# Performance work log

Measured on AMD Instinct MI355X. Metric: run time of the kernel, lower is better.

Reference implementation:

```python
import jax, jax.numpy as jnp
import numpy as np

# config constants
B, S, H = 4, 2048, 1024
E = 8                 # n_routed_experts
M = 512               # moe_intermediate_size
K = 2                 # num_experts_per_tok
N_SHARED = 2
SM = M * N_SHARED     # shared expert intermediate
G = 64                # gene_size
GE_TEMP = 1.0
ALPHA = 0.001         # aux_loss_alpha
SEQ_AUX = True
NORM_TOPK = True
COS_TEMP = 0.78
CONS_ALPHA = 0.01
LEAKY_SLOPE = 0.01
EPS_COS = 1e-8


def setup_inputs() -> dict:
    key = jax.random.key(0)
    ks = jax.random.split(key, 12)
    sh = 1.0 / np.sqrt(H)
    sm = 1.0 / np.sqrt(M)
    ssm = 1.0 / np.sqrt(SM)
    sg = 1.0 / np.sqrt(G)
    return {
        "hidden_states": jax.random.normal(ks[0], (B, S, H), jnp.float32),
        "g": jax.random.normal(ks[1], (B, G), jnp.float32),
        "wt": jax.random.uniform(ks[2], (E, H), jnp.float32, -sh, sh),   # gate weight_token
        "wg": jax.random.uniform(ks[3], (E, G), jnp.float32, -sg, sg),   # gate weight_gene
        "w_gate": jax.random.uniform(ks[4], (E, H, M), jnp.float32, -sh, sh),
        "w_up": jax.random.uniform(ks[5], (E, H, M), jnp.float32, -sh, sh),
        "w_down": jax.random.uniform(ks[6], (E, M, H), jnp.float32, -sm, sm),
        "sw_gate": jax.random.uniform(ks[7], (H, SM), jnp.float32, -sh, sh),
        "sw_up": jax.random.uniform(ks[8], (H, SM), jnp.float32, -sh, sh),
        "sw_down": jax.random.uniform(ks[9], (SM, H), jnp.float32, -ssm, ssm),
    }


def _leaky(x):
    return jnp.where(x >= 0, x, LEAKY_SLOPE * x)


def _moe_forward(hidden_states, g, wt, wg, w_gate, w_up, w_down, sw_gate, sw_up, sw_down):
    b, s, h = hidden_states.shape
    x = hidden_states.reshape(-1, h)                    # [T, H], T = b*s
    T = x.shape[0]

    # ---- gate ----
    logits_h = x @ wt.T                                 # [T, E]
    logits_g = g @ wg.T                                 # [b, E]
    logits_g = jnp.repeat(logits_g, s, axis=0)          # [T, E]
    logits = (logits_h + logits_g / GE_TEMP) / (1.0 + 1.0 / GE_TEMP)
    scores = jax.nn.softmax(logits, axis=-1)            # [T, E]
    topk_w, topk_idx = jax.lax.top_k(scores, K)         # [T, K]
    if K > 1 and NORM_TOPK:
        topk_w = topk_w / (topk_w.sum(-1, keepdims=True) + 1e-20)

    # aux loss (seq_aux=True)
    onehot = jax.nn.one_hot(topk_idx.reshape(b, s * K), E, dtype=jnp.float32)  # [b, s*K, E]
    ce = onehot.sum(1) / (s * K / E)                    # [b, E]
    aux_loss = (ce * scores.reshape(b, s, E).mean(1)).sum(1).mean() * ALPHA

    # ---- routed experts: dense stacked compute, then gather ----
    gp = _leaky(jnp.einsum('th,ehm->etm', x, w_gate))   # [E, T, M]
    up = jnp.einsum('th,ehm->etm', x, w_up)
    y_all = jnp.einsum('etm,emh->eth', gp * up, w_down) # [E, T, H]
    y_sel = y_all[topk_idx, jnp.arange(T)[:, None], :]  # [T, K, H]
    y = (y_sel * topk_w[..., None]).sum(1).reshape(b, s, h)

    # ---- shared expert ----
    p = (_leaky(hidden_states @ sw_gate) * (hidden_states @ sw_up)) @ sw_down
    y = y + p

    # consistency cosine loss
    num = jnp.sum(y * p, -1)
    den = jnp.maximum(jnp.linalg.norm(y, axis=-1), EPS_COS) * jnp.maximum(jnp.linalg.norm(p, axis=-1), EPS_COS)
    closs = CONS_ALPHA * jnp.mean((num / den) / (1.0 + COS_TEMP))
    return y, aux_loss + closs


def reference(hidden_states, g, wt, wg, w_gate, w_up, w_down, sw_gate, sw_up, sw_down):
    y, _ = _moe_forward(hidden_states, g, wt, wg, w_gate, w_up, w_down, sw_gate, sw_up, sw_down)
    return y
```

## Files before the change

### kernel.cpp

```cpp
#include <hip/hip_runtime.h>
#include <stdint.h>

#define T_TOK 8192
#define H_DIM 1024
#define M_DIM 512
#define SM_DIM 1024
#define E_NUM 8
#define S_SEQ 2048
#define G_DIM 64
#define NASSIGN 16384
#define NSLOT (NASSIGN + E_NUM * 256)
#define MAX_TILES (NASSIGN / 256 + E_NUM)
#define NBLK_PLACE (NASSIGN / 256)

typedef float f32x4 __attribute__((ext_vector_type(4)));
typedef short bf16x8 __attribute__((ext_vector_type(8)));

struct TileDesc { int base; int expert; int nrows; };

#define WAITCNT_VM6 asm volatile("s_waitcnt vmcnt(6)" ::: "memory")
#define WAITCNT_VM4 asm volatile("s_waitcnt vmcnt(4)" ::: "memory")
#define WAITCNT_VM2 asm volatile("s_waitcnt vmcnt(2)" ::: "memory")
#define WAITCNT_VM0 asm volatile("s_waitcnt vmcnt(0)" ::: "memory")
#define WAITCNT_LGKM0 asm volatile("s_waitcnt lgkmcnt(0)" ::: "memory")

static __device__ __forceinline__ ushort f2b(float f) {
  union { float f; uint32_t u; } a; a.f = f;
  uint32_t r = a.u + 0x7fffu + ((a.u >> 16) & 1u);
  return (ushort)(r >> 16);
}
static __device__ __forceinline__ float b2f(ushort u) {
  union { uint32_t u; float f; } a; a.u = ((uint32_t)u) << 16;
  return a.f;
}
static __device__ __forceinline__ int imin(int a, int b) { return a < b ? a : b; }

static __device__ __forceinline__ void gll16(const void* g, void* l) {
  __builtin_amdgcn_global_load_lds(
      (const __attribute__((address_space(1))) void*)g,
      (__attribute__((address_space(3))) void*)l, 16, 0, 0);
}
static __device__ __forceinline__ int xcd_remap(int wg, int nwg) {
  return (wg & 7) * (nwg >> 3) + (wg >> 3);
}

__global__ void cvt_x_kernel(const float* __restrict__ x, ushort* __restrict__ xb) {
  int i = blockIdx.x * 256 + threadIdx.x;
  const float4 v = ((const float4*)x)[i];
  ushort4 o;
  o.x = f2b(v.x); o.y = f2b(v.y); o.z = f2b(v.z); o.w = f2b(v.w);
  ((ushort4*)xb)[i] = o;
}

__global__ void tcvt_kernel(const float* __restrict__ src, ushort* __restrict__ dst, int R, int C) {
  __shared__ float tile[32][33];
  size_t bo = (size_t)blockIdx.z * R * C;
  src += bo; dst += bo;
  int c0 = blockIdx.x * 32, r0 = blockIdx.y * 32;
#pragma unroll
  for (int i = 0; i < 4; ++i)
    tile[threadIdx.y + i * 8][threadIdx.x] =
        src[(size_t)(r0 + threadIdx.y + i * 8) * C + c0 + threadIdx.x];
  __syncthreads();
#pragma unroll
  for (int i = 0; i < 4; ++i)
    dst[(size_t)(c0 + threadIdx.y + i * 8) * R + r0 + threadIdx.x] =
        f2b(tile[threadIdx.x][threadIdx.y + i * 8]);
}

__global__ void lg_kernel(const float* __restrict__ g, const float* __restrict__ wg,
                          float* __restrict__ lg) {
  int tid = threadIdx.x;
  if (tid < 4 * E_NUM) {
    int b = tid >> 3, e = tid & 7;
    float s = 0.f;
    for (int i = 0; i < G_DIM; ++i) s += g[b * G_DIM + i] * wg[e * G_DIM + i];
    lg[tid] = s;
  }
}

__global__ __launch_bounds__(64) void router_kernel(
    const float* __restrict__ x, const float* __restrict__ wt, const float* __restrict__ lg,
    int* __restrict__ tidx, float* __restrict__ tw) {
  int t = blockIdx.x;
  int lane = threadIdx.x;
  const float* xr = x + (size_t)t * H_DIM;
  float a[E_NUM];
#pragma unroll
  for (int e = 0; e < E_NUM; ++e) a[e] = 0.f;
  for (int i = lane; i < H_DIM; i += 64) {
    float xv = xr[i];
#pragma unroll
    for (int e = 0; e < E_NUM; ++e) a[e] += xv * wt[e * H_DIM + i];
  }
#pragma unroll
  for (int e = 0; e < E_NUM; ++e)
    for (int off = 32; off; off >>= 1) a[e] += __shfl_xor(a[e], off, 64);
  if (lane == 0) {
    int b = t / S_SEQ;
    float l[E_NUM];
#pragma unroll
    for (int e = 0; e < E_NUM; ++e) l[e] = 0.5f * (a[e] + lg[b * E_NUM + e]);
    int i1 = 0; float b1 = l[0];
#pragma unroll
    for (int e = 1; e < E_NUM; ++e) if (l[e] > b1) { b1 = l[e]; i1 = e; }
    int i2 = -1; float b2 = -1e30f;
#pragma unroll
    for (int e = 0; e < E_NUM; ++e) if (e != i1 && l[e] > b2) { b2 = l[e]; i2 = e; }
    float e2 = expf(b2 - b1);
    float inv = 1.f / (1.f + e2);
    tidx[t * 2] = i1; tidx[t * 2 + 1] = i2;
    tw[t * 2] = inv;  tw[t * 2 + 1] = e2 * inv;
  }
}

__global__ __launch_bounds__(256) void hist_kernel(const int* __restrict__ tidx,
                                                   int* __restrict__ bcount) {
  __shared__ int h[E_NUM];
  int tid = threadIdx.x;
  if (tid < E_NUM) h[tid] = 0;
  __syncthreads();
  atomicAdd(&h[tidx[blockIdx.x * 256 + tid]], 1);
  __syncthreads();
  if (tid < E_NUM) bcount[blockIdx.x * E_NUM + tid] = h[tid];
}

__global__ __launch_bounds__(64) void scan2_kernel(
    const int* __restrict__ bcount, int* __restrict__ boffs, int* __restrict__ offs,
    TileDesc* __restrict__ desc, int* __restrict__ ndesc) {
  __shared__ int cnt[E_NUM];
  __shared__ int off_s[E_NUM];
  int lane = threadIdx.x;
  if (lane < E_NUM) {
    int s = 0;
    for (int b = 0; b < NBLK_PLACE; ++b) s += bcount[b * E_NUM + lane];
    cnt[lane] = s;
  }
  __syncthreads();
  if (lane == 0) {
    int o = 0, nd = 0;
    for (int e = 0; e < E_NUM; ++e) {
      off_s[e] = o;
      offs[e] = o;
      int n = cnt[e];
      for (int tb = 0; tb < n; tb += 256) {
        desc[nd].base = o + tb; desc[nd].expert = e;
        desc[nd].nrows = imin(n - tb, 256);
        ++nd;
      }
      o += n;
    }
    offs[E_NUM] = o;
    *ndesc = nd;
  }
  __syncthreads();
  if (lane < E_NUM) {
    int run = off_s[lane];
    for (int b = 0; b < NBLK_PLACE; ++b) {
      boffs[b * E_NUM + lane] = run;
      run += bcount[b * E_NUM + lane];
    }
  }
}

__global__ __launch_bounds__(256) void place2_kernel(
    const int* __restrict__ tidx, const int* __restrict__ boffs,
    int* __restrict__ perm, int* __restrict__ slot_of) {
  __shared__ int wcnt[4][E_NUM];
  int tid = threadIdx.x, wv = tid >> 6, lane = tid & 63;
  int i = blockIdx.x * 256 + tid;
  int e = tidx[i];
  unsigned long long lower = (lane == 63) ? 0x7fffffffffffffffull : ((1ull << lane) - 1ull);
  int rank = 0;
#pragma unroll
  for (int ee = 0; ee < E_NUM; ++ee) {
    unsigned long long m = __ballot(e == ee);
    if (e == ee) rank = __popcll(m & lower);
    if (lane == 0) wcnt[wv][ee] = __popcll(m);
  }
  __syncthreads();
  int off = boffs[blockIdx.x * E_NUM + e];
  for (int w = 0; w < wv; ++w) off += wcnt[w][e];
  int pos = off + rank;
  perm[pos] = i >> 1;
  slot_of[i] = pos;
}

template <int DUAL>
static __device__ __forceinline__ void gemm_core8(
    const ushort* __restrict__ A, const ushort* __restrict__ B0,
    const ushort* __restrict__ B1, void* __restrict__ Out, int outf32,
    int Kd, int NdOut, int rowbase, int nrows, int n0,
    const int* __restrict__ perm, ushort* __restrict__ LDS) {
  int tid = threadIdx.x, wv = tid >> 6, lane = tid & 63;
  int wr = wv >> 2, wc = wv & 3;
  int lr = lane & 15, cg = lane >> 4;
  int sid = lane >> 3, dch = lane & 7;

  const ushort* apA[2][2];
  const ushort* apB[2][2];
#pragma unroll
  for (int qm = 0; qm < 2; ++qm)
#pragma unroll
    for (int k = 0; k < 2; ++k) {
      int idx = k * 64 + wv * 8 + sid;
      int gch = dch ^ (idx & 7);
      int grow = (idx >> 6) * 128 + qm * 64 + (idx & 63);
      grow = imin(grow, nrows - 1);
      int arow = perm ? perm[rowbase + grow] : rowbase + grow;
      apA[qm][k] = A + (size_t)arow * Kd + gch * 8;
    }
#pragma unroll
  for (int qn = 0; qn < 2; ++qn)
#pragma unroll
    for (int k = 0; k < 2; ++k) {
      int idx = k * 64 + wv * 8 + sid;
      int gch = dch ^ (idx & 7);
      int vrow = n0 + (idx >> 5) * 64 + qn * 32 + (idx & 31);
      const ushort* src; int brow;
      if (DUAL) {
        src = ((vrow >> 4) & 1) ? B1 : B0;
        brow = (vrow >> 5) * 16 + (vrow & 15);
      } else {
        src = B0; brow = vrow;
      }
      apB[qn][k] = src + (size_t)brow * Kd + gch * 8;
    }

  auto stgA = [&](int qm, int k, int nd) {
    gll16(apA[qm][k], LDS + nd * 16384 + qm * 8192 + (k * 512 + wv * 64) * 8);
    apA[qm][k] += 64;
  };
  auto stgB = [&](int qn, int k, int nd) {
    gll16(apB[qn][k], LDS + 32768 + nd * 16384 + qn * 8192 + (k * 512 + wv * 64) * 8);
    apB[qn][k] += 64;
  };
  auto rdA = [&](int d, int qm, int m, int kk) -> bf16x8 {
    int idx = wr * 64 + m * 16 + lr;
    int ch = (kk * 4 + cg) ^ (idx & 7);
    return *(const bf16x8*)(LDS + d * 16384 + qm * 8192 + idx * 64 + ch * 8);
  };
  auto rdB = [&](int d, int qn, int n, int kk) -> bf16x8 {
    int idx = wc * 32 + n * 16 + lr;
    int ch = (kk * 4 + cg) ^ (idx & 7);
    return *(const bf16x8*)(LDS + 32768 + d * 16384 + qn * 8192 + idx * 64 + ch * 8);
  };

  f32x4 acc[2][2][4][2];
#pragma unroll
  for (int qm = 0; qm < 2; ++qm)
#pragma unroll
    for (int qn = 0; qn < 2; ++qn)
#pragma unroll
      for (int m = 0; m < 4; ++m)
#pragma unroll
        for (int n = 0; n < 2; ++n) acc[qm][qn][m][n] = (f32x4){0.f, 0.f, 0.f, 0.f};

  int nk = Kd >> 6;
  stgA(0, 0, 0); stgA(0, 1, 0);
  stgB(0, 0, 0); stgB(0, 1, 0);
  stgB(1, 0, 0); stgB(1, 1, 0);
  stgA(1, 0, 0); stgA(1, 1, 0);
  WAITCNT_VM4;
  __builtin_amdgcn_s_barrier();

  for (int t = 0; t < nk; ++t) {
    int cur = t & 1, nxt = cur ^ 1;
    bool hn = (t + 1 < nk);
    bf16x8 a0f[4][2], a1f[4][2], b0f[2][2], b1f[2][2];

#pragma unroll
    for (int m = 0; m < 4; ++m) { a0f[m][0] = rdA(cur, 0, m, 0); a0f[m][1] = rdA(cur, 0, m, 1); }
#pragma unroll
    for (int n = 0; n < 2; ++n) { b0f[n][0] = rdB(cur, 0, n, 0); b0f[n][1] = rdB(cur, 0, n, 1); }
    if (hn) { stgA(0, 0, nxt); stgA(0, 1, nxt); WAITCNT_VM4; } else { WAITCNT_VM2; }
    WAITCNT_LGKM0;
    __builtin_amdgcn_s_barrier();
    __builtin_amdgcn_s_setprio(1);
#pragma unroll
    for (int m = 0; m < 4; ++m)
#pragma unroll
      for (int n = 0; n < 2; ++n) {
        acc[0][0][m][n] = __builtin_amdgcn_mfma_f32_16x16x32_bf16(a0f[m][0], b0f[n][0], acc[0][0][m][n], 0, 0, 0);
        acc[0][0][m][n] = __builtin_amdgcn_mfma_f32_16x16x32_bf16(a0f[m][1], b0f[n][1], acc[0][0][m][n], 0, 0, 0);
      }
    __builtin_amdgcn_s_setprio(0);

#pragma unroll
    for (int n = 0; n < 2; ++n) { b1f[n][0] = rdB(cur, 1, n, 0); b1f[n][1] = rdB(cur, 1, n, 1); }
    if (hn) { stgB(0, 0, nxt); stgB(0, 1, nxt); WAITCNT_VM4; } else { WAITCNT_VM0; }
    WAITCNT_LGKM0;
    __builtin_amdgcn_s_barrier();
    __builtin_amdgcn_s_setprio(1);
#pragma unroll
    for (int m = 0; m < 4; ++m)
#pragma unroll
      for (int n = 0; n < 2; ++n) {
        acc[0][1][m][n] = __builtin_amdgcn_mfma_f32_16x16x32_bf16(a0f[m][0], b1f[n][0], acc[0][1][m][n], 0, 0, 0);
        acc[0][1][m][n] = __builtin_amdgcn_mfma_f32_16x16x32_bf16(a0f[m][1], b1f[n][1], acc[0][1][m][n], 0, 0, 0);
      }
    __builtin_amdgcn_s_setprio(0);

#pragma unroll
    for (int m = 0; m < 4; ++m) { a1f[m][0] = rdA(cur, 1, m, 0); a1f[m][1] = rdA(cur, 1, m, 1); }
    if (hn) { stgB(1, 0, nxt); stgB(1, 1, nxt); WAITCNT_VM6; }
    WAITCNT_LGKM0;
    __builtin_amdgcn_s_barrier();
    __builtin_amdgcn_s_setprio(1);
#pragma unroll
    for (int m = 0; m < 4; ++m)
#pragma unroll
      for (int n = 0; n < 2; ++n) {
        acc[1][0][m][n] = __builtin_amdgcn_mfma_f32_16x16x32_bf16(a1f[m][0], b0f[n][0], acc[1][0][m][n], 0, 0, 0);
        acc[1][0][m][n] = __builtin_amdgcn_mfma_f32_16x16x32_bf16(a1f[m][1], b0f[n][1], acc[1][0][m][n], 0, 0, 0);
      }
    __builtin_amdgcn_s_setprio(0);

    if (hn) { stgA(1, 0, nxt); stgA(1, 1, nxt); WAITCNT_VM4; }
    WAITCNT_LGKM0;
    __builtin_amdgcn_s_barrier();
    __builtin_amdgcn_s_setprio(1);
#pragma unroll
    for (int m = 0; m < 4; ++m)
#pragma unroll
      for (int n = 0; n < 2; ++n) {
        acc[1][1][m][n] = __builtin_amdgcn_mfma_f32_16x16x32_bf16(a1f[m][0], b1f[n][0], acc[1][1][m][n], 0, 0, 0);
        acc[1][1][m][n] = __builtin_amdgcn_mfma_f32_16x16x32_bf16(a1f[m][1], b1f[n][1], acc[1][1][m][n], 0, 0, 0);
      }
    __builtin_amdgcn_s_setprio(0);
  }

#pragma unroll
  for (int qm = 0; qm < 2; ++qm)
#pragma unroll
    for (int qn = 0; qn < 2; ++qn)
#pragma unroll
      for (int m = 0; m < 4; ++m)
#pragma unroll
        for (int r = 0; r < 4; ++r) {
          int row = wr * 128 + qm * 64 + m * 16 + cg * 4 + r;
          if (row < nrows) {
            if (DUAL) {
              float gv = acc[qm][qn][m][0][r], uv = acc[qm][qn][m][1][r];
              float hv = (gv >= 0.f ? gv : 0.01f * gv) * uv;
              int col = ((n0 >> 5) + wc * 2 + qn) * 16 + lr;
              ((ushort*)Out)[(size_t)(rowbase + row) * NdOut + col] = f2b(hv);
            } else {
#pragma unroll
              for (int n = 0; n < 2; ++n) {
                int col = n0 + wc * 64 + qn * 32 + n * 16 + lr;
                size_t o = (size_t)(rowbase + row) * NdOut + col;
                if (outf32) ((float*)Out)[o] = acc[qm][qn][m][n][r];
                else ((ushort*)Out)[o] = f2b(acc[qm][qn][m][n][r]);
              }
            }
          }
        }
}

__global__ __launch_bounds__(512) void gemm_dual_all(
    const ushort* __restrict__ xb, const ushort* __restrict__ swg,
    const ushort* __restrict__ swu, ushort* __restrict__ hsh,
    const ushort* __restrict__ wg, const ushort* __restrict__ wu,
    ushort* __restrict__ h_e, const int* __restrict__ perm,
    const TileDesc* __restrict__ desc, const int* __restrict__ ndesc) {
  __shared__ ushort LDS[65536];
  int id = xcd_remap(blockIdx.x, gridDim.x);
  if (id < 256) {
    int mt = id >> 3, n0 = (id & 7) * 256;
    gemm_core8<1>(xb, swg, swu, hsh, 0, H_DIM, SM_DIM, mt * 256, 256, n0, nullptr, LDS);
  } else {
    int rid = id - 256;
    int mt = rid >> 2, n0 = (rid & 3) * 256;
    if (mt >= *ndesc) return;
    TileDesc d = desc[mt];
    size_t wo = (size_t)d.expert * M_DIM * H_DIM;
    gemm_core8<1>(xb, wg + wo, wu + wo, h_e, 0, H_DIM, M_DIM, d.base, d.nrows, n0, perm, LDS);
  }
}

__global__ __launch_bounds__(512) void gemm_down_all(
    const ushort* __restrict__ hsh, const ushort* __restrict__ swd, float* __restrict__ y,
    const ushort* __restrict__ h_e, const ushort* __restrict__ wd, ushort* __restrict__ ye,
    const TileDesc* __restrict__ desc, const int* __restrict__ ndesc) {
  __shared__ ushort LDS[65536];
  int id = xcd_remap(blockIdx.x, gridDim.x);
  if (id < 128) {
    int mt = id >> 2, n0 = (id & 3) * 256;
    gemm_core8<0>(hsh, swd, nullptr, (void*)y, 1, SM_DIM, H_DIM, mt * 256, 256, n0, nullptr, LDS);
  } else {
    int rid = id - 128;
    int mt = rid >> 2, n0 = (rid & 3) * 256;
    if (mt >= *ndesc) return;
    TileDesc d = desc[mt];
    gemm_core8<0>(h_e, wd + (size_t)d.expert * H_DIM * M_DIM, nullptr, (void*)ye, 0,
                  M_DIM, H_DIM, d.base, d.nrows, n0, nullptr, LDS);
  }
}

__global__ void final_kernel(float* __restrict__ y, const ushort* __restrict__ ye,
                             const int* __restrict__ slot_of, const float* __restrict__ tw) {
  int i = blockIdx.x * 256 + threadIdx.x;
  int t = i >> 8;
  int c4 = (i & 255) * 4;
  int s0 = slot_of[t * 2], s1 = slot_of[t * 2 + 1];
  float w0 = tw[t * 2], w1 = tw[t * 2 + 1];
  float4 v = ((float4*)y)[i];
  ushort4 a = *(const ushort4*)(ye + (size_t)s0 * H_DIM + c4);
  ushort4 b = *(const ushort4*)(ye + (size_t)s1 * H_DIM + c4);
  v.x += w0 * b2f(a.x) + w1 * b2f(b.x);
  v.y += w0 * b2f(a.y) + w1 * b2f(b.y);
  v.z += w0 * b2f(a.z) + w1 * b2f(b.z);
  v.w += w0 * b2f(a.w) + w1 * b2f(b.w);
  ((float4*)y)[i] = v;
}

extern "C" void kernel_launch(void* const* d_in, const int* in_sizes, int n_in,
                              void* d_out, int out_size, void* d_ws, size_t ws_size,
                              hipStream_t stream) {
  const float* x       = (const float*)d_in[0];
  const float* g       = (const float*)d_in[1];
  const float* wt      = (const float*)d_in[2];
  const float* wg      = (const float*)d_in[3];
  const float* w_gate  = (const float*)d_in[4];
  const float* w_up    = (const float*)d_in[5];
  const float* w_down  = (const float*)d_in[6];
  const float* sw_gate = (const float*)d_in[7];
  const float* sw_up   = (const float*)d_in[8];
  const float* sw_down = (const float*)d_in[9];
  float* y = (float*)d_out;

  char* p = (char*)d_ws;
  auto alloc = [&](size_t bytes) -> char* {
    char* r = p;
    p += (bytes + 255) & ~(size_t)255;
    return r;
  };
  ushort* xb    = (ushort*)alloc((size_t)T_TOK * H_DIM * 2);
  ushort* wg_t  = (ushort*)alloc((size_t)E_NUM * M_DIM * H_DIM * 2);
  ushort* wu_t  = (ushort*)alloc((size_t)E_NUM * M_DIM * H_DIM * 2);
  ushort* wd_t  = (ushort*)alloc((size_t)E_NUM * H_DIM * M_DIM * 2);
  ushort* swg_t = (ushort*)alloc((size_t)SM_DIM * H_DIM * 2);
  ushort* swu_t = (ushort*)alloc((size_t)SM_DIM * H_DIM * 2);
  ushort* swd_t = (ushort*)alloc((size_t)H_DIM * SM_DIM * 2);
  float* lg     = (float*)alloc(4 * E_NUM * 4);
  int* tidx     = (int*)alloc(NASSIGN * 4);
  float* tw     = (float*)alloc(NASSIGN * 4);
  int* bcount   = (int*)alloc(NBLK_PLACE * E_NUM * 4);
  int* boffs    = (int*)alloc(NBLK_PLACE * E_NUM * 4);
  int* offs     = (int*)alloc((E_NUM + 1) * 4);
  int* ndesc    = (int*)alloc(4);
  int* perm     = (int*)alloc(NASSIGN * 4);
  int* slot_of  = (int*)alloc(NASSIGN * 4);
  TileDesc* desc = (TileDesc*)alloc(MAX_TILES * sizeof(TileDesc));
  ushort* h_e   = (ushort*)alloc((size_t)NSLOT * M_DIM * 2);
  ushort* hsh   = (ushort*)alloc((size_t)T_TOK * SM_DIM * 2);
  ushort* ye    = (ushort*)alloc((size_t)NSLOT * H_DIM * 2);
  (void)ws_size; (void)in_sizes; (void)n_in; (void)out_size;

  cvt_x_kernel<<<T_TOK * H_DIM / 4 / 256, 256, 0, stream>>>(x, xb);
  dim3 tb(32, 8);
  tcvt_kernel<<<dim3(M_DIM / 32, H_DIM / 32, E_NUM), tb, 0, stream>>>(w_gate, wg_t, H_DIM, M_DIM);
  tcvt_kernel<<<dim3(M_DIM / 32, H_DIM / 32, E_NUM), tb, 0, stream>>>(w_up, wu_t, H_DIM, M_DIM);
  tcvt_kernel<<<dim3(H_DIM / 32, M_DIM / 32, E_NUM), tb, 0, stream>>>(w_down, wd_t, M_DIM, H_DIM);
  tcvt_kernel<<<dim3(SM_DIM / 32, H_DIM / 32, 1), tb, 0, stream>>>(sw_gate, swg_t, H_DIM, SM_DIM);
  tcvt_kernel<<<dim3(SM_DIM / 32, H_DIM / 32, 1), tb, 0, stream>>>(sw_up, swu_t, H_DIM, SM_DIM);
  tcvt_kernel<<<dim3(H_DIM / 32, SM_DIM / 32, 1), tb, 0, stream>>>(sw_down, swd_t, SM_DIM, H_DIM);

  lg_kernel<<<1, 32, 0, stream>>>(g, wg, lg);
  router_kernel<<<T_TOK, 64, 0, stream>>>(x, wt, lg, tidx, tw);
  hist_kernel<<<NBLK_PLACE, 256, 0, stream>>>(tidx, bcount);
  scan2_kernel<<<1, 64, 0, stream>>>(bcount, boffs, offs, desc, ndesc);
  place2_kernel<<<NBLK_PLACE, 256, 0, stream>>>(tidx, boffs, perm, slot_of);

  gemm_dual_all<<<256 + MAX_TILES * 4, 512, 0, stream>>>(
      xb, swg_t, swu_t, hsh, wg_t, wu_t, h_e, perm, desc, ndesc);
  gemm_down_all<<<128 + MAX_TILES * 4, 512, 0, stream>>>(
      hsh, swd_t, y, h_e, wd_t, ye, desc, ndesc);

  final_kernel<<<T_TOK * H_DIM / 4 / 256, 256, 0, stream>>>(y, ye, slot_of, tw);
}
```

Before: 222.2 us.

## Fuse weight/x conversion and routing into one prep kernel, bf16 shared output

Merges the six weight transpose-convert launches, the x-to-bf16 conversion, the gene-logit kernel and the router into a single prep kernel. The router now reads x once with float4 loads and writes the bf16 copy in the same pass. The shared-expert down projection now writes a bf16 buffer instead of the fp32 output. The final kernel uses a grid-stride loop to sum the shared and routed results and write y. This cuts launch overhead and the extra fp32 read-modify-write of y, at the cost of rounding the shared-expert output to bf16 and recomputing the gene logits in every wave.

```diff
diff --git a/kernel.cpp b/kernel.cpp
--- a/kernel.cpp
+++ b/kernel.cpp
@@ -44,63 +44,76 @@
   return (wg & 7) * (nwg >> 3) + (wg >> 3);
 }
 
-__global__ void cvt_x_kernel(const float* __restrict__ x, ushort* __restrict__ xb) {
-  int i = blockIdx.x * 256 + threadIdx.x;
-  const float4 v = ((const float4*)x)[i];
-  ushort4 o;
-  o.x = f2b(v.x); o.y = f2b(v.y); o.z = f2b(v.z); o.w = f2b(v.w);
-  ((ushort4*)xb)[i] = o;
-}
-
-__global__ void tcvt_kernel(const float* __restrict__ src, ushort* __restrict__ dst, int R, int C) {
+__global__ __launch_bounds__(256) void prep_kernel(
+    const float* __restrict__ x, const float* __restrict__ wt, const float* __restrict__ g,
+    const float* __restrict__ wgm,
+    const float* __restrict__ w_gate, const float* __restrict__ w_up,
+    const float* __restrict__ w_down, const float* __restrict__ sw_gate,
+    const float* __restrict__ sw_up, const float* __restrict__ sw_down,
+    ushort* __restrict__ wg_t, ushort* __restrict__ wu_t,
+    ushort* __restrict__ wd_t, ushort* __restrict__ swg_t,
+    ushort* __restrict__ swu_t, ushort* __restrict__ swd_t,
+    ushort* __restrict__ xb, int* __restrict__ tidx, float* __restrict__ tw) {
   __shared__ float tile[32][33];
-  size_t bo = (size_t)blockIdx.z * R * C;
-  src += bo; dst += bo;
-  int c0 = blockIdx.x * 32, r0 = blockIdx.y * 32;
-#pragma unroll
-  for (int i = 0; i < 4; ++i)
-    tile[threadIdx.y + i * 8][threadIdx.x] =
-        src[(size_t)(r0 + threadIdx.y + i * 8) * C + c0 + threadIdx.x];
-  __syncthreads();
-#pragma unroll
-  for (int i = 0; i < 4; ++i)
-    dst[(size_t)(c0 + threadIdx.y + i * 8) * R + r0 + threadIdx.x] =
-        f2b(tile[threadIdx.x][threadIdx.y + i * 8]);
-}
-
-__global__ void lg_kernel(const float* __restrict__ g, const float* __restrict__ wg,
-                          float* __restrict__ lg) {
-  int tid = threadIdx.x;
-  if (tid < 4 * E_NUM) {
-    int b = tid >> 3, e = tid & 7;
-    float s = 0.f;
-    for (int i = 0; i < G_DIM; ++i) s += g[b * G_DIM + i] * wg[e * G_DIM + i];
-    lg[tid] = s;
-  }
-}
-
-__global__ __launch_bounds__(64) void router_kernel(
-    const float* __restrict__ x, const float* __restrict__ wt, const float* __restrict__ lg,
-    int* __restrict__ tidx, float* __restrict__ tw) {
-  int t = blockIdx.x;
-  int lane = threadIdx.x;
-  const float* xr = x + (size_t)t * H_DIM;
+  int id = blockIdx.x;
+  if (id < 15360) {
+    int tx = threadIdx.x & 31, ty = threadIdx.x >> 5;
+    const float* src; ushort* dst; int R, C, t;
+    if (id < 4096)        { src = w_gate;  dst = wg_t;  R = 1024; C = 512;  t = id; }
+    else if (id < 8192)   { src = w_up;    dst = wu_t;  R = 1024; C = 512;  t = id - 4096; }
+    else if (id < 12288)  { src = w_down;  dst = wd_t;  R = 512;  C = 1024; t = id - 8192; }
+    else if (id < 13312)  { src = sw_gate; dst = swg_t; R = 1024; C = 1024; t = id - 12288; }
+    else if (id < 14336)  { src = sw_up;   dst = swu_t; R = 1024; C = 1024; t = id - 13312; }
+    else                  { src = sw_down; dst = swd_t; R = 1024; C = 1024; t = id - 14336; }
+    int tc = C >> 5;
+    int tpm = (R >> 5) * tc;
+    int e = t / tpm, tt = t % tpm;
+    int c0 = (tt % tc) * 32, r0 = (tt / tc) * 32;
+    size_t bo = (size_t)e * R * C;
+    src += bo; dst += bo;
+#pragma unroll
+    for (int i = 0; i < 4; ++i)
+      tile[ty + i * 8][tx] = src[(size_t)(r0 + ty + i * 8) * C + c0 + tx];
+    __syncthreads();
+#pragma unroll
+    for (int i = 0; i < 4; ++i)
+      dst[(size_t)(c0 + ty + i * 8) * R + r0 + tx] = f2b(tile[tx][ty + i * 8]);
+    return;
+  }
+  int id2 = id - 15360;
+  int wv = threadIdx.x >> 6, lane = threadIdx.x & 63;
+  int t = id2 * 4 + wv;
+  const float4* xr4 = (const float4*)x + (size_t)t * 256;
+  ushort4* xb4 = (ushort4*)xb + (size_t)t * 256;
   float a[E_NUM];
 #pragma unroll
   for (int e = 0; e < E_NUM; ++e) a[e] = 0.f;
-  for (int i = lane; i < H_DIM; i += 64) {
-    float xv = xr[i];
-#pragma unroll
-    for (int e = 0; e < E_NUM; ++e) a[e] += xv * wt[e * H_DIM + i];
+#pragma unroll
+  for (int j = 0; j < 4; ++j) {
+    float4 v = xr4[lane + 64 * j];
+    ushort4 o;
+    o.x = f2b(v.x); o.y = f2b(v.y); o.z = f2b(v.z); o.w = f2b(v.w);
+    xb4[lane + 64 * j] = o;
+#pragma unroll
+    for (int e = 0; e < E_NUM; ++e) {
+      float4 wv4 = ((const float4*)(wt + (size_t)e * H_DIM))[lane + 64 * j];
+      a[e] += v.x * wv4.x + v.y * wv4.y + v.z * wv4.z + v.w * wv4.w;
+    }
   }
 #pragma unroll
   for (int e = 0; e < E_NUM; ++e)
     for (int off = 32; off; off >>= 1) a[e] += __shfl_xor(a[e], off, 64);
+  float lge = 0.f;
+  int b = t / S_SEQ;
+  if (lane < E_NUM) {
+    const float* gv = g + b * G_DIM;
+    const float* wv2 = wgm + lane * G_DIM;
+    for (int i = 0; i < G_DIM; ++i) lge += gv[i] * wv2[i];
+  }
+  float l[E_NUM];
+#pragma unroll
+  for (int e = 0; e < E_NUM; ++e) l[e] = 0.5f * (a[e] + __shfl(lge, e, 64));
   if (lane == 0) {
-    int b = t / S_SEQ;
-    float l[E_NUM];
-#pragma unroll
-    for (int e = 0; e < E_NUM; ++e) l[e] = 0.5f * (a[e] + lg[b * E_NUM + e]);
     int i1 = 0; float b1 = l[0];
 #pragma unroll
     for (int e = 1; e < E_NUM; ++e) if (l[e] > b1) { b1 = l[e]; i1 = e; }
@@ -380,14 +393,14 @@
 }
 
 __global__ __launch_bounds__(512) void gemm_down_all(
-    const ushort* __restrict__ hsh, const ushort* __restrict__ swd, float* __restrict__ y,
+    const ushort* __restrict__ hsh, const ushort* __restrict__ swd, ushort* __restrict__ ysh,
     const ushort* __restrict__ h_e, const ushort* __restrict__ wd, ushort* __restrict__ ye,
     const TileDesc* __restrict__ desc, const int* __restrict__ ndesc) {
   __shared__ ushort LDS[65536];
   int id = xcd_remap(blockIdx.x, gridDim.x);
   if (id < 128) {
     int mt = id >> 2, n0 = (id & 3) * 256;
-    gemm_core8<0>(hsh, swd, nullptr, (void*)y, 1, SM_DIM, H_DIM, mt * 256, 256, n0, nullptr, LDS);
+    gemm_core8<0>(hsh, swd, nullptr, (void*)ysh, 0, SM_DIM, H_DIM, mt * 256, 256, n0, nullptr, LDS);
   } else {
     int rid = id - 128;
     int mt = rid >> 2, n0 = (rid & 3) * 256;
@@ -398,21 +411,24 @@
   }
 }
 
-__global__ void final_kernel(float* __restrict__ y, const ushort* __restrict__ ye,
-                             const int* __restrict__ slot_of, const float* __restrict__ tw) {
-  int i = blockIdx.x * 256 + threadIdx.x;
-  int t = i >> 8;
-  int c4 = (i & 255) * 4;
-  int s0 = slot_of[t * 2], s1 = slot_of[t * 2 + 1];
-  float w0 = tw[t * 2], w1 = tw[t * 2 + 1];
-  float4 v = ((float4*)y)[i];
-  ushort4 a = *(const ushort4*)(ye + (size_t)s0 * H_DIM + c4);
-  ushort4 b = *(const ushort4*)(ye + (size_t)s1 * H_DIM + c4);
-  v.x += w0 * b2f(a.x) + w1 * b2f(b.x);
-  v.y += w0 * b2f(a.y) + w1 * b2f(b.y);
-  v.z += w0 * b2f(a.z) + w1 * b2f(b.z);
-  v.w += w0 * b2f(a.w) + w1 * b2f(b.w);
-  ((float4*)y)[i] = v;
+__global__ __launch_bounds__(256) void final_kernel(
+    float* __restrict__ y, const ushort* __restrict__ ysh, const ushort* __restrict__ ye,
+    const int* __restrict__ slot_of, const float* __restrict__ tw) {
+  for (int i = blockIdx.x * 256 + threadIdx.x; i < T_TOK * H_DIM / 4; i += 2048 * 256) {
+    int t = i >> 8;
+    int c4 = (i & 255) * 4;
+    int s0 = slot_of[t * 2], s1 = slot_of[t * 2 + 1];
+    float w0 = tw[t * 2], w1 = tw[t * 2 + 1];
+    ushort4 pp = *(const ushort4*)(ysh + (size_t)t * H_DIM + c4);
+    ushort4 a = *(const ushort4*)(ye + (size_t)s0 * H_DIM + c4);
+    ushort4 b = *(const ushort4*)(ye + (size_t)s1 * H_DIM + c4);
+    float4 v;
+    v.x = b2f(pp.x) + w0 * b2f(a.x) + w1 * b2f(b.x);
+    v.y = b2f(pp.y) + w0 * b2f(a.y) + w1 * b2f(b.y);
+    v.z = b2f(pp.z) + w0 * b2f(a.z) + w1 * b2f(b.z);
+    v.w = b2f(pp.w) + w0 * b2f(a.w) + w1 * b2f(b.w);
+    ((float4*)y)[i] = v;
+  }
 }
 
 extern "C" void kernel_launch(void* const* d_in, const int* in_sizes, int n_in,
@@ -443,7 +459,6 @@
   ushort* swg_t = (ushort*)alloc((size_t)SM_DIM * H_DIM * 2);
   ushort* swu_t = (ushort*)alloc((size_t)SM_DIM * H_DIM * 2);
   ushort* swd_t = (ushort*)alloc((size_t)H_DIM * SM_DIM * 2);
-  float* lg     = (float*)alloc(4 * E_NUM * 4);
   int* tidx     = (int*)alloc(NASSIGN * 4);
   float* tw     = (float*)alloc(NASSIGN * 4);
   int* bcount   = (int*)alloc(NBLK_PLACE * E_NUM * 4);
@@ -456,19 +471,12 @@
   ushort* h_e   = (ushort*)alloc((size_t)NSLOT * M_DIM * 2);
   ushort* hsh   = (ushort*)alloc((size_t)T_TOK * SM_DIM * 2);
   ushort* ye    = (ushort*)alloc((size_t)NSLOT * H_DIM * 2);
+  ushort* ysh   = (ushort*)alloc((size_t)T_TOK * H_DIM * 2);
   (void)ws_size; (void)in_sizes; (void)n_in; (void)out_size;
 
-  cvt_x_kernel<<<T_TOK * H_DIM / 4 / 256, 256, 0, stream>>>(x, xb);
-  dim3 tb(32, 8);
-  tcvt_kernel<<<dim3(M_DIM / 32, H_DIM / 32, E_NUM), tb, 0, stream>>>(w_gate, wg_t, H_DIM, M_DIM);
-  tcvt_kernel<<<dim3(M_DIM / 32, H_DIM / 32, E_NUM), tb, 0, stream>>>(w_up, wu_t, H_DIM, M_DIM);
-  tcvt_kernel<<<dim3(H_DIM / 32, M_DIM / 32, E_NUM), tb, 0, stream>>>(w_down, wd_t, M_DIM, H_DIM);
-  tcvt_kernel<<<dim3(SM_DIM / 32, H_DIM / 32, 1), tb, 0, stream>>>(sw_gate, swg_t, H_DIM, SM_DIM);
-  tcvt_kernel<<<dim3(SM_DIM / 32, H_DIM / 32, 1), tb, 0, stream>>>(sw_up, swu_t, H_DIM, SM_DIM);
-  tcvt_kernel<<<dim3(H_DIM / 32, SM_DIM / 32, 1), tb, 0, stream>>>(sw_down, swd_t, SM_DIM, H_DIM);
-
-  lg_kernel<<<1, 32, 0, stream>>>(g, wg, lg);
-  router_kernel<<<T_TOK, 64, 0, stream>>>(x, wt, lg, tidx, tw);
+  prep_kernel<<<15360 + 2048, 256, 0, stream>>>(
+      x, wt, g, wg, w_gate, w_up, w_down, sw_gate, sw_up, sw_down,
+      wg_t, wu_t, wd_t, swg_t, swu_t, swd_t, xb, tidx, tw);
   hist_kernel<<<NBLK_PLACE, 256, 0, stream>>>(tidx, bcount);
   scan2_kernel<<<1, 64, 0, stream>>>(bcount, boffs, offs, desc, ndesc);
   place2_kernel<<<NBLK_PLACE, 256, 0, stream>>>(tidx, boffs, perm, slot_of);
@@ -476,7 +484,7 @@
   gemm_dual_all<<<256 + MAX_TILES * 4, 512, 0, stream>>>(
       xb, swg_t, swu_t, hsh, wg_t, wu_t, h_e, perm, desc, ndesc);
   gemm_down_all<<<128 + MAX_TILES * 4, 512, 0, stream>>>(
-      hsh, swd_t, y, h_e, wd_t, ye, desc, ndesc);
-
-  final_kernel<<<T_TOK * H_DIM / 4 / 256, 256, 0, stream>>>(y, ye, slot_of, tw);
-}
+      hsh, swd_t, ysh, h_e, wd_t, ye, desc, ndesc);
+
+  final_kernel<<<2048, 256, 0, stream>>>(y, ysh, ye, slot_of, tw);
+}
```

After: 207.5 us. -6.6%, faster.
